# Optimization experiments

Measured on AMD Instinct MI355X. Metric: run time of the kernel, lower is better.

The kernel has to match this reference:

```python
import jax, jax.numpy as jnp
import numpy as np

BETA = 0.1
NUM_PTVS = 3  # labels 1..3; 0 = background


def setup_inputs() -> dict:
    key = jax.random.key(0)
    k1, k2, k3, k4 = jax.random.split(key, 4)
    shape = (8, 128, 128, 128)
    return {
        "predicted_dose": jax.random.uniform(k1, shape, dtype=jnp.float32),
        "target_dose": jax.random.uniform(k2, shape, dtype=jnp.float32),
        "PTV_mask_batch": jax.random.randint(k3, shape, 0, NUM_PTVS + 1, dtype=jnp.int32),
        "ptv_values": jax.random.uniform(k4, (NUM_PTVS,), dtype=jnp.float32),
    }


def _structure_dvh(dose, mask, ptv_values):
    # dose: [B, D, H, W] float, mask: [B, D, H, W] int in {0..K}
    # Fused single-pass version of the nested-loop torch code: each voxel's
    # sigmoid only contributes to its own structure, so we can look up the
    # per-voxel threshold and segment-sum by label.
    B = dose.shape[0]
    K = ptv_values.shape[0]
    d = dose.reshape(B, -1)          # [B, V]
    m = mask.reshape(B, -1)          # [B, V]
    thr = ptv_values[jnp.clip(m - 1, 0)]            # [B, V]; background dummy-indexed, masked out below
    sig = jax.nn.sigmoid((d - thr) / BETA)          # [B, V]
    seg_sum = jax.vmap(lambda s, l: jax.ops.segment_sum(s, l, num_segments=K + 1))(sig, m)  # [B, K+1]
    seg_cnt = jax.vmap(lambda l: jax.ops.segment_sum(jnp.ones(l.shape, dtype=sig.dtype), l, num_segments=K + 1))(m)
    return seg_sum[:, 1:] / seg_cnt[:, 1:]          # [B, K], drop background label 0


def reference(predicted_dose, target_dose, PTV_mask_batch, ptv_values):
    pred_dvh = _structure_dvh(predicted_dose, PTV_mask_batch, ptv_values)
    targ_dvh = _structure_dvh(target_dose, PTV_mask_batch, ptv_values)
    return jnp.mean((pred_dvh - targ_dvh) ** 2)
```

## Files before the change

kernel.cpp:

```cpp
#include <hip/hip_runtime.h>


#define NB 8
#define NK 3
#define VPB (1 << 21)
#define BLOCK 256
#define CHUNKS 512
#define NBLOCKS (NB * CHUNKS)
#define VOX_PER_BLOCK (VPB / CHUNKS)

#define WS_PARTIALS (6 * NBLOCKS)

#define LOG2E_X10 14.4269504088896341f

typedef float v4f __attribute__((ext_vector_type(4)));
typedef int   v4i __attribute__((ext_vector_type(4)));

__global__ __launch_bounds__(BLOCK) void dvh_sum_kernel(
    const float* __restrict__ pred,
    const float* __restrict__ targ,
    const int*   __restrict__ mask,
    const float* __restrict__ ptv,
    double*      __restrict__ ws)
{
    const int bid   = blockIdx.x;
    const int batch = bid / CHUNKS;
    const int chunk = bid % CHUNKS;
    const long base = (long)batch * VPB + (long)chunk * VOX_PER_BLOCK;

    const float* predb = pred + base;
    const float* targb = targ + base;
    const int*   maskb = mask + base;

    const int tid = threadIdx.x;
    const unsigned off0 = (unsigned)(tid) * 16u;
    const unsigned off1 = (unsigned)(tid + BLOCK) * 16u;
    const unsigned off2 = (unsigned)(tid + 2 * BLOCK) * 16u;
    const unsigned off3 = (unsigned)(tid + 3 * BLOCK) * 16u;

    v4f P0, P1, P2, P3, T0, T1, T2, T3;
    v4i M0, M1, M2, M3;

    asm volatile(
        "global_load_dwordx4 %0,  %12, %16\n\t"
        "global_load_dwordx4 %1,  %13, %16\n\t"
        "global_load_dwordx4 %2,  %14, %16\n\t"
        "global_load_dwordx4 %3,  %15, %16\n\t"
        "global_load_dwordx4 %4,  %12, %17\n\t"
        "global_load_dwordx4 %5,  %13, %17\n\t"
        "global_load_dwordx4 %6,  %14, %17\n\t"
        "global_load_dwordx4 %7,  %15, %17\n\t"
        "global_load_dwordx4 %8,  %12, %18\n\t"
        "global_load_dwordx4 %9,  %13, %18\n\t"
        "global_load_dwordx4 %10, %14, %18\n\t"
        "global_load_dwordx4 %11, %15, %18\n\t"
        "s_waitcnt vmcnt(0)"
        : "=&v"(P0), "=&v"(P1), "=&v"(P2), "=&v"(P3),
          "=&v"(T0), "=&v"(T1), "=&v"(T2), "=&v"(T3),
          "=&v"(M0), "=&v"(M1), "=&v"(M2), "=&v"(M3)
        : "v"(off0), "v"(off1), "v"(off2), "v"(off3),
          "s"(predb), "s"(targb), "s"(maskb));

    const float tc0 = ptv[0] * LOG2E_X10;
    const float tc1 = ptv[1] * LOG2E_X10;
    const float tc2 = ptv[2] * LOG2E_X10;

    float d0 = 0.f, d1 = 0.f, d2 = 0.f;
    int   c0 = 0,   c1 = 0,   c2 = 0;

    #define DO_ELEM(PJ, TJ, MJ)                                          \
    {                                                                    \
        const int mm = (MJ);                                             \
        const bool is1 = (mm == 1), is2 = (mm == 2), is3 = (mm == 3);    \
        const float thrC = is1 ? tc0 : (is2 ? tc1 : tc2);                \
        const float ep = __builtin_amdgcn_exp2f(                         \
                             __builtin_fmaf((PJ), -LOG2E_X10, thrC));    \
        const float et = __builtin_amdgcn_exp2f(                         \
                             __builtin_fmaf((TJ), -LOG2E_X10, thrC));    \
        const float sgp = __builtin_amdgcn_rcpf(1.0f + ep);              \
        const float sgt = __builtin_amdgcn_rcpf(1.0f + et);              \
        const float df  = sgp - sgt;                                     \
        d0 += is1 ? df : 0.0f;                                           \
        d1 += is2 ? df : 0.0f;                                           \
        d2 += is3 ? df : 0.0f;                                           \
        c0 += is1 ? 1 : 0;                                               \
        c1 += is2 ? 1 : 0;                                               \
        c2 += is3 ? 1 : 0;                                               \
    }

    #define DO_VEC4(P, T, M)                                             \
        DO_ELEM(P[0], T[0], M[0])                                        \
        DO_ELEM(P[1], T[1], M[1])                                        \
        DO_ELEM(P[2], T[2], M[2])                                        \
        DO_ELEM(P[3], T[3], M[3])

    DO_VEC4(P0, T0, M0)
    DO_VEC4(P1, T1, M1)
    DO_VEC4(P2, T2, M2)
    DO_VEC4(P3, T3, M3)
    #undef DO_VEC4
    #undef DO_ELEM

    #pragma unroll
    for (int off = 32; off > 0; off >>= 1) {
        d0 += __shfl_down(d0, off, 64);
        d1 += __shfl_down(d1, off, 64);
        d2 += __shfl_down(d2, off, 64);
        c0 += __shfl_down(c0, off, 64);
        c1 += __shfl_down(c1, off, 64);
        c2 += __shfl_down(c2, off, 64);
    }

    __shared__ double redd[BLOCK / 64][3];
    __shared__ int    redc[BLOCK / 64][3];
    const int wid  = threadIdx.x >> 6;
    const int lane = threadIdx.x & 63;
    if (lane == 0) {
        redd[wid][0] = (double)d0; redd[wid][1] = (double)d1; redd[wid][2] = (double)d2;
        redc[wid][0] = c0;         redc[wid][1] = c1;         redc[wid][2] = c2;
    }
    __syncthreads();

    if (threadIdx.x < 6) {
        const int q = threadIdx.x;
        double s;
        if (q < 3)
            s = redd[0][q] + redd[1][q] + redd[2][q] + redd[3][q];
        else
            s = (double)(redc[0][q - 3] + redc[1][q - 3] + redc[2][q - 3] + redc[3][q - 3]);
        ws[(size_t)q * NBLOCKS + bid] = s;
    }
}

__global__ __launch_bounds__(64) void dvh_reduce_kernel(
    const double* __restrict__ ws, double* __restrict__ ws2)
{
    const int j = blockIdx.x;
    const int b = j / NK, k = j % NK;
    const double* dp = ws + (size_t)k * NBLOCKS + b * CHUNKS;
    const double* cp = ws + (size_t)(NK + k) * NBLOCKS + b * CHUNKS;

    double sd = 0.0, sc = 0.0;
    #pragma unroll
    for (int i = threadIdx.x; i < CHUNKS; i += 64) {
        sd += dp[i];
        sc += cp[i];
    }
    #pragma unroll
    for (int off = 32; off > 0; off >>= 1) {
        sd += __shfl_down(sd, off, 64);
        sc += __shfl_down(sc, off, 64);
    }
    if (threadIdx.x == 0) {
        const double d = sd / sc;
        ws2[j] = d * d;
    }
}

__global__ __launch_bounds__(64) void dvh_out_kernel(
    const double* __restrict__ ws2, float* __restrict__ out)
{
    double v = (threadIdx.x < NB * NK) ? ws2[threadIdx.x] : 0.0;
    #pragma unroll
    for (int off = 32; off > 0; off >>= 1)
        v += __shfl_down(v, off, 64);
    if (threadIdx.x == 0) out[0] = (float)(v / (double)(NB * NK));
}

extern "C" void kernel_launch(void* const* d_in, const int* in_sizes, int n_in,
                              void* d_out, int out_size, void* d_ws, size_t ws_size,
                              hipStream_t stream) {
    const float* pred = (const float*)d_in[0];
    const float* targ = (const float*)d_in[1];
    const int*   mask = (const int*)d_in[2];
    const float* ptv  = (const float*)d_in[3];
    float* out = (float*)d_out;
    double* ws  = (double*)d_ws;
    double* ws2 = ws + WS_PARTIALS;

    dvh_sum_kernel<<<NBLOCKS, BLOCK, 0, stream>>>(pred, targ, mask, ptv, ws);
    dvh_reduce_kernel<<<NB * NK, 64, 0, stream>>>(ws, ws2);
    dvh_out_kernel<<<1, 64, 0, stream>>>(ws2, out);
}
```

Measured before the change: 41.47 us.

## Interleave loads with staged waitcnts and fuse final reductions into one kernel

The load order is changed so that each vector group's pred, targ and mask arrive together. Staged s_waitcnt instructions then let computation on early groups overlap with the remaining loads. The two small reduction kernels are merged into a single one-block finalize kernel, removing a launch. Per-block partials are now stored as float sums and int counts rather than doubles, which shrinks workspace traffic but slightly lowers the precision of the block partials.

New measurement: 42.18 us. Within noise of the previous version (+1.7%).

```diff
diff --git a/kernel.cpp b/kernel.cpp
--- a/kernel.cpp
+++ b/kernel.cpp
@@ -9,8 +9,6 @@
 #define NBLOCKS (NB * CHUNKS)
 #define VOX_PER_BLOCK (VPB / CHUNKS)
 
-#define WS_PARTIALS (6 * NBLOCKS)
-
 #define LOG2E_X10 14.4269504088896341f
 
 typedef float v4f __attribute__((ext_vector_type(4)));
@@ -21,7 +19,8 @@
     const float* __restrict__ targ,
     const int*   __restrict__ mask,
     const float* __restrict__ ptv,
-    double*      __restrict__ ws)
+    float*       __restrict__ wsd,
+    int*         __restrict__ wsc)
 {
     const int bid   = blockIdx.x;
     const int batch = bid / CHUNKS;
@@ -38,32 +37,33 @@
     const unsigned off2 = (unsigned)(tid + 2 * BLOCK) * 16u;
     const unsigned off3 = (unsigned)(tid + 3 * BLOCK) * 16u;
 
+    const float tc0 = ptv[0] * LOG2E_X10;
+    const float tc1 = ptv[1] * LOG2E_X10;
+    const float tc2 = ptv[2] * LOG2E_X10;
+
     v4f P0, P1, P2, P3, T0, T1, T2, T3;
     v4i M0, M1, M2, M3;
 
     asm volatile(
         "global_load_dwordx4 %0,  %12, %16\n\t"
-        "global_load_dwordx4 %1,  %13, %16\n\t"
-        "global_load_dwordx4 %2,  %14, %16\n\t"
-        "global_load_dwordx4 %3,  %15, %16\n\t"
-        "global_load_dwordx4 %4,  %12, %17\n\t"
-        "global_load_dwordx4 %5,  %13, %17\n\t"
-        "global_load_dwordx4 %6,  %14, %17\n\t"
-        "global_load_dwordx4 %7,  %15, %17\n\t"
-        "global_load_dwordx4 %8,  %12, %18\n\t"
-        "global_load_dwordx4 %9,  %13, %18\n\t"
-        "global_load_dwordx4 %10, %14, %18\n\t"
-        "global_load_dwordx4 %11, %15, %18\n\t"
-        "s_waitcnt vmcnt(0)"
-        : "=&v"(P0), "=&v"(P1), "=&v"(P2), "=&v"(P3),
-          "=&v"(T0), "=&v"(T1), "=&v"(T2), "=&v"(T3),
-          "=&v"(M0), "=&v"(M1), "=&v"(M2), "=&v"(M3)
+        "global_load_dwordx4 %1,  %12, %17\n\t"
+        "global_load_dwordx4 %2,  %12, %18\n\t"
+        "global_load_dwordx4 %3,  %13, %16\n\t"
+        "global_load_dwordx4 %4,  %13, %17\n\t"
+        "global_load_dwordx4 %5,  %13, %18\n\t"
+        "global_load_dwordx4 %6,  %14, %16\n\t"
+        "global_load_dwordx4 %7,  %14, %17\n\t"
+        "global_load_dwordx4 %8,  %14, %18\n\t"
+        "global_load_dwordx4 %9,  %15, %16\n\t"
+        "global_load_dwordx4 %10, %15, %17\n\t"
+        "global_load_dwordx4 %11, %15, %18"
+        : "=&v"(P0), "=&v"(T0), "=&v"(M0),
+          "=&v"(P1), "=&v"(T1), "=&v"(M1),
+          "=&v"(P2), "=&v"(T2), "=&v"(M2),
+          "=&v"(P3), "=&v"(T3), "=&v"(M3)
         : "v"(off0), "v"(off1), "v"(off2), "v"(off3),
-          "s"(predb), "s"(targb), "s"(maskb));
-
-    const float tc0 = ptv[0] * LOG2E_X10;
-    const float tc1 = ptv[1] * LOG2E_X10;
-    const float tc2 = ptv[2] * LOG2E_X10;
+          "s"(predb), "s"(targb), "s"(maskb),
+          "v"(tc0), "v"(tc1), "v"(tc2));
 
     float d0 = 0.f, d1 = 0.f, d2 = 0.f;
     int   c0 = 0,   c1 = 0,   c2 = 0;
@@ -94,9 +94,13 @@
         DO_ELEM(P[2], T[2], M[2])                                        \
         DO_ELEM(P[3], T[3], M[3])
 
+    asm volatile("s_waitcnt vmcnt(9)" : "+v"(P0), "+v"(T0), "+v"(M0));
     DO_VEC4(P0, T0, M0)
+    asm volatile("s_waitcnt vmcnt(6)" : "+v"(P1), "+v"(T1), "+v"(M1));
     DO_VEC4(P1, T1, M1)
+    asm volatile("s_waitcnt vmcnt(3)" : "+v"(P2), "+v"(T2), "+v"(M2));
     DO_VEC4(P2, T2, M2)
+    asm volatile("s_waitcnt vmcnt(0)" : "+v"(P3), "+v"(T3), "+v"(M3));
     DO_VEC4(P3, T3, M3)
     #undef DO_VEC4
     #undef DO_ELEM
@@ -111,60 +115,68 @@
         c2 += __shfl_down(c2, off, 64);
     }
 
-    __shared__ double redd[BLOCK / 64][3];
-    __shared__ int    redc[BLOCK / 64][3];
+    __shared__ float redd[BLOCK / 64][3];
+    __shared__ int   redc[BLOCK / 64][3];
     const int wid  = threadIdx.x >> 6;
     const int lane = threadIdx.x & 63;
     if (lane == 0) {
-        redd[wid][0] = (double)d0; redd[wid][1] = (double)d1; redd[wid][2] = (double)d2;
-        redc[wid][0] = c0;         redc[wid][1] = c1;         redc[wid][2] = c2;
+        redd[wid][0] = d0; redd[wid][1] = d1; redd[wid][2] = d2;
+        redc[wid][0] = c0; redc[wid][1] = c1; redc[wid][2] = c2;
     }
     __syncthreads();
 
     if (threadIdx.x < 6) {
         const int q = threadIdx.x;
-        double s;
         if (q < 3)
-            s = redd[0][q] + redd[1][q] + redd[2][q] + redd[3][q];
+            wsd[(size_t)q * NBLOCKS + bid] =
+                redd[0][q] + redd[1][q] + redd[2][q] + redd[3][q];
         else
-            s = (double)(redc[0][q - 3] + redc[1][q - 3] + redc[2][q - 3] + redc[3][q - 3]);
-        ws[(size_t)q * NBLOCKS + bid] = s;
+            wsc[(size_t)(q - 3) * NBLOCKS + bid] =
+                redc[0][q - 3] + redc[1][q - 3] + redc[2][q - 3] + redc[3][q - 3];
     }
 }
 
-__global__ __launch_bounds__(64) void dvh_reduce_kernel(
-    const double* __restrict__ ws, double* __restrict__ ws2)
+__global__ __launch_bounds__(256) void dvh_finalize_kernel(
+    const float* __restrict__ wsd,
+    const int*   __restrict__ wsc,
+    float*       __restrict__ out)
 {
-    const int j = blockIdx.x;
-    const int b = j / NK, k = j % NK;
-    const double* dp = ws + (size_t)k * NBLOCKS + b * CHUNKS;
-    const double* cp = ws + (size_t)(NK + k) * NBLOCKS + b * CHUNKS;
+    const int tid  = threadIdx.x;
+    const int wave = tid >> 6;
+    const int lane = tid & 63;
 
-    double sd = 0.0, sc = 0.0;
-    #pragma unroll
-    for (int i = threadIdx.x; i < CHUNKS; i += 64) {
-        sd += dp[i];
-        sc += cp[i];
+    __shared__ double lds[NB * NK];
+
+    for (int j = wave; j < NB * NK; j += 4) {
+        const int b = j / NK, k = j % NK;
+        const float* dp = wsd + (size_t)k * NBLOCKS + b * CHUNKS;
+        const int*   cp = wsc + (size_t)k * NBLOCKS + b * CHUNKS;
+
+        double sd = 0.0;
+        int    sc = 0;
+        #pragma unroll
+        for (int i = lane; i < CHUNKS; i += 64) {
+            sd += (double)dp[i];
+            sc += cp[i];
+        }
+        #pragma unroll
+        for (int off = 32; off > 0; off >>= 1) {
+            sd += __shfl_down(sd, off, 64);
+            sc += __shfl_down(sc, off, 64);
+        }
+        if (lane == 0) {
+            const double d = sd / (double)sc;
+            lds[j] = d * d;
+        }
     }
-    #pragma unroll
-    for (int off = 32; off > 0; off >>= 1) {
-        sd += __shfl_down(sd, off, 64);
-        sc += __shfl_down(sc, off, 64);
+    __syncthreads();
+
+    if (tid == 0) {
+        double t = 0.0;
+        #pragma unroll
+        for (int j = 0; j < NB * NK; ++j) t += lds[j];
+        out[0] = (float)(t / (double)(NB * NK));
     }
-    if (threadIdx.x == 0) {
-        const double d = sd / sc;
-        ws2[j] = d * d;
-    }
-}
-
-__global__ __launch_bounds__(64) void dvh_out_kernel(
-    const double* __restrict__ ws2, float* __restrict__ out)
-{
-    double v = (threadIdx.x < NB * NK) ? ws2[threadIdx.x] : 0.0;
-    #pragma unroll
-    for (int off = 32; off > 0; off >>= 1)
-        v += __shfl_down(v, off, 64);
-    if (threadIdx.x == 0) out[0] = (float)(v / (double)(NB * NK));
 }
 
 extern "C" void kernel_launch(void* const* d_in, const int* in_sizes, int n_in,
@@ -175,10 +187,10 @@
     const int*   mask = (const int*)d_in[2];
     const float* ptv  = (const float*)d_in[3];
     float* out = (float*)d_out;
-    double* ws  = (double*)d_ws;
-    double* ws2 = ws + WS_PARTIALS;
 
-    dvh_sum_kernel<<<NBLOCKS, BLOCK, 0, stream>>>(pred, targ, mask, ptv, ws);
-    dvh_reduce_kernel<<<NB * NK, 64, 0, stream>>>(ws, ws2);
-    dvh_out_kernel<<<1, 64, 0, stream>>>(ws2, out);
+    float* wsd = (float*)d_ws;
+    int*   wsc = (int*)(wsd + 3 * NBLOCKS);
+
+    dvh_sum_kernel<<<NBLOCKS, BLOCK, 0, stream>>>(pred, targ, mask, ptv, wsd, wsc);
+    dvh_finalize_kernel<<<1, 256, 0, stream>>>(wsd, wsc, out);
 }
```
